# Kernel optimization log

Hardware: AMD Instinct MI355X
Metric: run time of the kernel (lower is better)

## Reference

```python
import jax, jax.numpy as jnp
import numpy as np

B, C, H, W = 8, 192, 56, 56
K = 9          # kernel_size (k nearest neighbors), dilation=1
G = 4          # conv groups in BasicConv
EPS_BN = 1e-5


def setup_inputs() -> dict:
    key = jax.random.key(0)
    ks = jax.random.split(key, 5)
    C2 = 2 * C
    gi = C2 // G
    x = jax.random.normal(ks[0], (B, C, H, W), jnp.float32)
    # fc1: Conv2d(C,C,1) + BN(C)
    w_fc1 = jax.random.normal(ks[1], (C, C), jnp.float32) * (1.0 / np.sqrt(C))
    b_fc1 = jnp.zeros((C,), jnp.float32)
    g_fc1 = jnp.ones((C,), jnp.float32)
    be_fc1 = jnp.zeros((C,), jnp.float32)
    # graph conv BasicConv: grouped Conv2d(2C,2C,1,groups=4) + BN(2C) + GELU
    w_gc = jax.random.normal(ks[2], (C2, gi), jnp.float32) * np.sqrt(2.0 / gi)  # kaiming
    b_gc = jnp.zeros((C2,), jnp.float32)
    g_gc = jnp.ones((C2,), jnp.float32)
    be_gc = jnp.zeros((C2,), jnp.float32)
    # fc2: Conv2d(2C,C,1) + BN(C)
    w_fc2 = jax.random.normal(ks[3], (C, C2), jnp.float32) * (1.0 / np.sqrt(C2))
    b_fc2 = jnp.zeros((C,), jnp.float32)
    g_fc2 = jnp.ones((C,), jnp.float32)
    be_fc2 = jnp.zeros((C,), jnp.float32)
    return dict(x=x, w_fc1=w_fc1, b_fc1=b_fc1, g_fc1=g_fc1, be_fc1=be_fc1,
                w_gc=w_gc, b_gc=b_gc, g_gc=g_gc, be_gc=be_gc,
                w_fc2=w_fc2, b_fc2=b_fc2, g_fc2=g_fc2, be_fc2=be_fc2)


def _bn(x, g, b):
    # training-mode BatchNorm over (batch, points) per channel; x: [B,N,C]
    mu = jnp.mean(x, axis=(0, 1))
    var = jnp.var(x, axis=(0, 1))  # biased, as torch BN uses for normalization
    return (x - mu) * jax.lax.rsqrt(var + EPS_BN) * g + b


def _forward(x, w_fc1, b_fc1, g_fc1, be_fc1, w_gc, b_gc, g_gc, be_gc,
             w_fc2, b_fc2, g_fc2, be_fc2):
    Bb, Cc, Hh, Ww = x.shape
    N = Hh * Ww
    x0 = x.reshape(Bb, Cc, N).transpose(0, 2, 1)          # [B,N,C]
    h = _bn(x0 @ w_fc1.T + b_fc1, g_fc1, be_fc1)          # fc1

    # --- dynamic kNN graph on L2-normalized features (no-grad in torch) ---
    f = jax.lax.stop_gradient(h)
    f = f / jnp.maximum(jnp.linalg.norm(f, axis=-1, keepdims=True), 1e-12)
    sq = jnp.sum(f * f, axis=-1, keepdims=True)           # [B,N,1]
    dist = sq - 2.0 * jnp.einsum('bnc,bmc->bnm', f, f) + sq.transpose(0, 2, 1)
    _, idx = jax.lax.top_k(-dist, K)                      # [B,N,K] neighbor indices

    # --- max-relative aggregation ---
    xj = h[jnp.arange(Bb)[:, None, None], idx]            # gather: [B,N,K,C]
    rel = jnp.max(xj - h[:, :, None, :], axis=2)          # [B,N,C]
    # interleave channels: c*2 + {0: h, 1: rel} (matches cat(dim=2).reshape)
    feat = jnp.stack([h, rel], axis=-1).reshape(Bb, N, 2 * Cc)

    # --- grouped 1x1 conv + BN + GELU ---
    C2 = 2 * Cc
    gi = C2 // G
    fg = feat.reshape(Bb, N, G, gi)
    wg = w_gc.reshape(G, gi, gi)                          # [group, out_pg, in_pg]
    y = jnp.einsum('bngi,goi->bngo', fg, wg).reshape(Bb, N, C2) + b_gc
    y = jax.nn.gelu(_bn(y, g_gc, be_gc), approximate=False)

    # --- fc2 + residual ---
    out = _bn(y @ w_fc2.T + b_fc2, g_fc2, be_fc2) + x0
    return out.transpose(0, 2, 1).reshape(Bb, Cc, Hh, Ww)


def reference(x, w_fc1, b_fc1, g_fc1, be_fc1, w_gc, b_gc, g_gc, be_gc,
              w_fc2, b_fc2, g_fc2, be_fc2):
    return _forward(x, w_fc1, b_fc1, g_fc1, be_fc1, w_gc, b_gc, g_gc, be_gc,
                    w_fc2, b_fc2, g_fc2, be_fc2)
```

## Files before the change

### kernel.cpp

```cpp
#include <hip/hip_runtime.h>
#include <math.h>

#define BB 8
#define CC 192
#define NN 3136
#define NR 25088
#define C2 384
#define GI 96
#define KNN 9
#define NCHUNK 256
#define RPC 98
#define EPS_BN 1e-5f

typedef unsigned short ushortT;
typedef unsigned int uintT;
typedef _Float16 f16x8 __attribute__((ext_vector_type(8)));
typedef float f32x4 __attribute__((ext_vector_type(4)));

static __device__ __forceinline__ ushortT f16b(_Float16 v) {
  union { _Float16 f; ushortT u; } x; x.f = v; return x.u;
}
static __device__ __forceinline__ float f16tof(ushortT u) {
  union { ushortT u; _Float16 f; } x; x.u = u; return (float)x.f;
}
static __device__ __forceinline__ float packdi(float d, int cidx) {
  return __uint_as_float((__float_as_uint(d) & 0xFFFFF800u) | (uintT)cidx);
}

__global__ __launch_bounds__(256) void k_fc1(const float* __restrict__ x,
        const float* __restrict__ w1, const float* __restrict__ b1,
        float* __restrict__ z) {
  __shared__ __align__(16) float Xs[32*68];
  __shared__ __align__(16) float Ws[32*68];
  int b = blockIdx.z, n0 = blockIdx.x*64, c0 = blockIdx.y*64;
  int tid = threadIdx.x;
  int tcol = tid & 15, trow = tid >> 4;
  float acc[4][4] = {};
  const float4* xf4 = (const float4*)x;
  const float4* wf4 = (const float4*)w1;
  for (int kb = 0; kb < 6; ++kb) {
    int k0 = kb*32;
    __syncthreads();
    #pragma unroll
    for (int s = 0; s < 2; ++s) {
      int q = tid + 256*s;
      int kk = q >> 4, nq = q & 15;
      ((float4*)Xs)[kk*17 + nq] = xf4[(size_t)(b*CC + k0 + kk)*784 + (n0>>2) + nq];
    }
    #pragma unroll
    for (int s = 0; s < 2; ++s) {
      int q = tid + 256*s;
      int cc = q >> 3, kq = q & 7;
      float4 v = wf4[(size_t)(c0 + cc)*48 + (k0>>2) + kq];
      Ws[(kq*4+0)*68 + cc] = v.x;
      Ws[(kq*4+1)*68 + cc] = v.y;
      Ws[(kq*4+2)*68 + cc] = v.z;
      Ws[(kq*4+3)*68 + cc] = v.w;
    }
    __syncthreads();
    #pragma unroll 8
    for (int kk = 0; kk < 32; ++kk) {
      float4 a4 = ((const float4*)Xs)[kk*17 + trow];
      float4 b4 = ((const float4*)Ws)[kk*17 + tcol];
      float av[4] = {a4.x,a4.y,a4.z,a4.w};
      float bv[4] = {b4.x,b4.y,b4.z,b4.w};
      #pragma unroll
      for (int i = 0; i < 4; ++i)
        #pragma unroll
        for (int j = 0; j < 4; ++j)
          acc[i][j] += av[i]*bv[j];
    }
  }
  float4 bias = ((const float4*)b1)[(c0>>2) + tcol];
  float bb4[4] = {bias.x,bias.y,bias.z,bias.w};
  #pragma unroll
  for (int i = 0; i < 4; ++i) {
    int n = n0 + trow*4 + i;
    float4 o;
    o.x = acc[i][0] + bb4[0]; o.y = acc[i][1] + bb4[1];
    o.z = acc[i][2] + bb4[2]; o.w = acc[i][3] + bb4[3];
    ((float4*)z)[(size_t)(b*NN + n)*48 + (c0>>2) + tcol] = o;
  }
}

__global__ void k_stats_part(const float* __restrict__ src, int C, float* __restrict__ part) {
  int c = threadIdx.x;
  int chunk = blockIdx.x;
  float s = 0.f, ss = 0.f;
  const float* p = src + (size_t)chunk*RPC*C + c;
  for (int r = 0; r < RPC; ++r) {
    float v = p[(size_t)r*C];
    s += v; ss += v*v;
  }
  part[(size_t)chunk*C + c] = s;
  part[(size_t)(NCHUNK + chunk)*C + c] = ss;
}

__global__ void k_stats_fin(const float* __restrict__ part, int C,
      const float* __restrict__ g, const float* __restrict__ be,
      float* __restrict__ scale, float* __restrict__ shift) {
  int c = threadIdx.x;
  float s = 0.f, ss = 0.f;
  for (int ch = 0; ch < NCHUNK; ++ch) {
    s  += part[(size_t)ch*C + c];
    ss += part[(size_t)(NCHUNK+ch)*C + c];
  }
  float mu = s / (float)NR;
  float var = ss/(float)NR - mu*mu;
  float rs = 1.0f / sqrtf(var + EPS_BN);
  float sc = g[c]*rs;
  scale[c] = sc;
  shift[c] = be[c] - mu*sc;
}

__global__ void k_packw(const float* __restrict__ src, int n4,
                        ushortT* __restrict__ hi, ushortT* __restrict__ lo) {
  int i = blockIdx.x*256 + threadIdx.x;
  if (i >= n4) return;
  float4 v = ((const float4*)src)[i];
  float vv[4] = {v.x, v.y, v.z, v.w};
  ushortT hb[4], lb[4];
  #pragma unroll
  for (int t = 0; t < 4; ++t) {
    _Float16 hh = (_Float16)vv[t];
    float r = vv[t] - (float)hh;
    _Float16 ll = (_Float16)(r*4096.f);
    hb[t] = f16b(hh); lb[t] = f16b(ll);
  }
  ((uint2*)hi)[i] = make_uint2((uintT)hb[0] | ((uintT)hb[1]<<16), (uintT)hb[2] | ((uintT)hb[3]<<16));
  ((uint2*)lo)[i] = make_uint2((uintT)lb[0] | ((uintT)lb[1]<<16), (uintT)lb[2] | ((uintT)lb[3]<<16));
}

__global__ __launch_bounds__(256) void k_h_f(float* __restrict__ h,
      ushortT* __restrict__ fhi, ushortT* __restrict__ flo, float* __restrict__ sqh,
      const float* __restrict__ scale, const float* __restrict__ shift) {
  __shared__ __align__(16) float fbuf[4][192];
  int w = threadIdx.x >> 6, lane = threadIdx.x & 63;
  size_t row = (size_t)blockIdx.x*4 + w;
  float* hp = h + row*CC;
  float hv[3]; float s = 0.f;
  #pragma unroll
  for (int t = 0; t < 3; ++t) {
    int c = lane + 64*t;
    float v = hp[c]*scale[c] + shift[c];
    hv[t] = v; s += v*v;
  }
  #pragma unroll
  for (int o = 32; o; o >>= 1) s += __shfl_xor(s, o);
  float eta = fmaxf(sqrtf(s), 1e-12f);
  float fv[3]; float s2 = 0.f;
  #pragma unroll
  for (int t = 0; t < 3; ++t) { fv[t] = hv[t]/eta; s2 += fv[t]*fv[t]; }
  #pragma unroll
  for (int o = 32; o; o >>= 1) s2 += __shfl_xor(s2, o);
  #pragma unroll
  for (int t = 0; t < 3; ++t) {
    int c = lane + 64*t;
    hp[c] = hv[t];
    fbuf[w][c] = fv[t];
  }
  if (lane == 0) sqh[row] = 0.5f*s2;
  __syncthreads();
  if (threadIdx.x < 192) {
    int r = threadIdx.x / 48, q = threadIdx.x % 48;
    size_t grow = (size_t)blockIdx.x*4 + r;
    float4 v = *(float4*)&fbuf[r][q*4];
    _Float16 a0=(_Float16)v.x, a1=(_Float16)v.y, a2=(_Float16)v.z, a3=(_Float16)v.w;
    float r0=v.x-(float)a0, r1=v.y-(float)a1, r2=v.z-(float)a2, r3=v.w-(float)a3;
    _Float16 b0=(_Float16)(r0*4096.f), b1=(_Float16)(r1*4096.f);
    _Float16 b2=(_Float16)(r2*4096.f), b3=(_Float16)(r3*4096.f);
    uintT hi0 = (uintT)f16b(a0) | ((uintT)f16b(a1)<<16);
    uintT hi1 = (uintT)f16b(a2) | ((uintT)f16b(a3)<<16);
    uintT lo0 = (uintT)f16b(b0) | ((uintT)f16b(b1)<<16);
    uintT lo1 = (uintT)f16b(b2) | ((uintT)f16b(b3)<<16);
    ((uint2*)(fhi + grow*CC))[q] = make_uint2(hi0, hi1);
    ((uint2*)(flo + grow*CC))[q] = make_uint2(lo0, lo1);
  }
}

__global__ __launch_bounds__(256) void k_knn12(const ushortT* __restrict__ fhi_,
    const float* __restrict__ sqh, int* __restrict__ idx12) {
  __shared__ __align__(16) f16x8 AHs[2][768];
  __shared__ float sqs[1568];
  int id = blockIdx.x;
  int b = id & 7, half = (id >> 3) & 1, rt = id >> 4;
  int tid = threadIdx.x, w = tid >> 6, lane = tid & 63;
  int l15 = lane & 15, kg = lane >> 4;

  const f16x8* FH = (const f16x8*)(fhi_ + (size_t)b*NN*CC);
  int cbase = half*1568;
  const f16x8* FC = FH + (size_t)cbase*24;

  int soff[3];
  #pragma unroll
  for (int i = 0; i < 3; ++i) {
    int s = i*256 + tid;
    int rr = s/24, u = s - rr*24;
    soff[i] = rr*24 + (u ^ (rr&7));
  }
  #pragma unroll
  for (int i = 0; i < 3; ++i)
    __builtin_amdgcn_global_load_lds(
      (const __attribute__((address_space(1))) void*)(FC + soff[i]),
      (__attribute__((address_space(3))) void*)&AHs[0][i*256 + w*64], 16, 0, 0);

  for (int i = tid; i < 1568/4; i += 256)
    ((float4*)sqs)[i] = ((const float4*)(sqh + (size_t)b*NN + cbase))[i];

  int row = rt*64 + w*16 + l15;
  f16x8 Bh[6];
  #pragma unroll
  for (int ks = 0; ks < 6; ++ks)
    Bh[ks] = FH[(size_t)row*24 + ks*4 + kg];

  float PD[12];
  #pragma unroll
  for (int t = 0; t < 12; ++t) PD[t] = -3.0e38f;

  __syncthreads();

  int buf = 0;
  for (int ct = 0; ct < 49; ++ct) {
    if (ct + 1 < 49) {
      #pragma unroll
      for (int i = 0; i < 3; ++i)
        __builtin_amdgcn_global_load_lds(
          (const __attribute__((address_space(1))) void*)(FC + (ct+1)*768 + soff[i]),
          (__attribute__((address_space(3))) void*)&AHs[buf^1][i*256 + w*64], 16, 0, 0);
    }
    f32x4 acc0 = {0.f,0.f,0.f,0.f}, acc1 = {0.f,0.f,0.f,0.f};
    #pragma unroll
    for (int ks = 0; ks < 6; ++ks) {
      int ub = ks*4 + kg;
      f16x8 a0 = AHs[buf][(     l15)*24 + (ub ^ (l15&7))];
      f16x8 a1 = AHs[buf][(16 + l15)*24 + (ub ^ (l15&7))];
      acc0 = __builtin_amdgcn_mfma_f32_16x16x32_f16(a0, Bh[ks], acc0, 0, 0, 0);
      acc1 = __builtin_amdgcn_mfma_f32_16x16x32_f16(a1, Bh[ks], acc1, 0, 0, 0);
    }
    int jbl = ct*32 + kg*4;
    float4 s0 = *(float4*)&sqs[jbl];
    float4 s1 = *(float4*)&sqs[jbl + 16];
    float dv[8] = {acc0[0]-s0.x, acc0[1]-s0.y, acc0[2]-s0.z, acc0[3]-s0.w,
                   acc1[0]-s1.x, acc1[1]-s1.y, acc1[2]-s1.z, acc1[3]-s1.w};
    #pragma unroll
    for (int r = 0; r < 8; ++r) {
      float dp = packdi(dv[r], jbl + (r&3) + ((r>>2)<<4));
      PD[0] = fmaxf(PD[0], dp);
      #pragma unroll
      for (int t = 0; t < 11; ++t) {
        float a = PD[t], c2 = PD[t+1];
        PD[t] = fminf(a, c2); PD[t+1] = fmaxf(a, c2);
      }
    }
    __syncthreads();
    buf ^= 1;
  }

  #pragma unroll
  for (int t = 0; t < 12; ++t) {
    float od = __shfl_xor(PD[t], 32);
    float od2 = (kg < 2) ? od : -3.0e38f;
    PD[0] = fmaxf(PD[0], od2);
    #pragma unroll
    for (int t2 = 0; t2 < 11; ++t2) {
      float a = PD[t2], c2 = PD[t2+1];
      PD[t2] = fminf(a, c2); PD[t2+1] = fmaxf(a, c2);
    }
  }
  #pragma unroll
  for (int t = 0; t < 12; ++t) {
    float od = __shfl_xor(PD[t], 16);
    float od2 = (kg == 0) ? od : -3.0e38f;
    PD[0] = fmaxf(PD[0], od2);
    #pragma unroll
    for (int t2 = 0; t2 < 11; ++t2) {
      float a = PD[t2], c2 = PD[t2+1];
      PD[t2] = fminf(a, c2); PD[t2+1] = fmaxf(a, c2);
    }
  }
  if (kg == 0) {
    size_t base = ((size_t)(b*NN + row)*2 + half)*12;
    #pragma unroll
    for (int t = 0; t < 12; ++t)
      idx12[base + t] = cbase + (int)(__float_as_uint(PD[t]) & 0x7FFu);
  }
}

__global__ __launch_bounds__(256) void k_refine(const ushortT* __restrict__ fhi_,
    const ushortT* __restrict__ flo_, const float* __restrict__ sqh,
    const int* __restrict__ idx12, int* __restrict__ idxg) {
  int id = blockIdx.x;
  int b = id & 7, rq = id >> 3;
  int w = threadIdx.x >> 6, lane = threadIdx.x & 63;
  int row = rq*4 + w;
  const ushortT* FHb = fhi_ + (size_t)b*NN*CC;
  const ushortT* FLb = flo_ + (size_t)b*NN*CC;
  float rv[3];
  #pragma unroll
  for (int t = 0; t < 3; ++t) {
    int c = lane + 64*t;
    rv[t] = f16tof(FHb[(size_t)row*CC + c]) + f16tof(FLb[(size_t)row*CC + c])*2.44140625e-4f;
  }
  const int* JP = idx12 + (size_t)(b*NN + row)*24;
  float TD[9]; int TI[9];
  #pragma unroll
  for (int t = 0; t < 9; ++t) { TD[t] = -3.0e38f; TI[t] = 0x7fffffff; }
  #pragma unroll
  for (int g = 0; g < 4; ++g) {
    int J6[6]; float s6[6];
    #pragma unroll
    for (int e = 0; e < 6; ++e) J6[e] = JP[g*6 + e];
    #pragma unroll
    for (int e = 0; e < 6; ++e) {
      int j = J6[e];
      float s = 0.f;
      #pragma unroll
      for (int t = 0; t < 3; ++t) {
        int c = lane + 64*t;
        float cv = f16tof(FHb[(size_t)j*CC + c]) + f16tof(FLb[(size_t)j*CC + c])*2.44140625e-4f;
        s = fmaf(rv[t], cv, s);
      }
      s6[e] = s;
    }
    #pragma unroll
    for (int o = 32; o; o >>= 1) {
      #pragma unroll
      for (int e = 0; e < 6; ++e) s6[e] += __shfl_xor(s6[e], o);
    }
    #pragma unroll
    for (int e = 0; e < 6; ++e) {
      int j = J6[e];
      float d = s6[e] - sqh[(size_t)b*NN + j];
      bool ins = (d > TD[0]) || (d == TD[0] && j < TI[0]);
      if (ins) {
        TD[0] = d; TI[0] = j;
        #pragma unroll
        for (int t = 0; t < 8; ++t) {
          bool sw = (TD[t] > TD[t+1]) || (TD[t] == TD[t+1] && TI[t] < TI[t+1]);
          if (sw) {
            float td = TD[t]; TD[t] = TD[t+1]; TD[t+1] = td;
            int ti = TI[t]; TI[t] = TI[t+1]; TI[t+1] = ti;
          }
        }
      }
    }
  }
  if (lane == 0) {
    size_t base = (size_t)(b*NN + row)*KNN;
    #pragma unroll
    for (int t = 0; t < KNN; ++t) idxg[base + t] = TI[t];
  }
}

__global__ __launch_bounds__(256) void k_gather(const float* __restrict__ h,
    const int* __restrict__ idxg, float* __restrict__ feat) {
  int w = threadIdx.x >> 6, lane = threadIdx.x & 63;
  size_t rg = (size_t)blockIdx.x*4 + w;
  int b = (int)(rg / NN);
  int n = (int)(rg % NN);
  const float* hb = h + (size_t)b*NN*CC;
  int j[KNN];
  #pragma unroll
  for (int t = 0; t < KNN; ++t) j[t] = idxg[rg*KNN + t];
  float2* featp = (float2*)feat;
  #pragma unroll
  for (int t = 0; t < 3; ++t) {
    int c = lane + 64*t;
    float self = hb[(size_t)n*CC + c];
    float m = -3.0e38f;
    #pragma unroll
    for (int k = 0; k < KNN; ++k) m = fmaxf(m, hb[(size_t)j[k]*CC + c]);
    featp[rg*CC + c] = make_float2(self, m - self);
  }
}

__global__ __launch_bounds__(256) void k_gconv(float* __restrict__ feat,
    const ushortT* __restrict__ wgh, const ushortT* __restrict__ wgl,
    const float* __restrict__ bgc, float* __restrict__ y) {
  int rt = blockIdx.x, g = blockIdx.y;
  int tid = threadIdx.x, w = tid >> 6, lane = tid & 63;
  int l15 = lane & 15, kg = lane >> 4;
  int row = rt*64 + w*16 + l15;
  const float4* F4 = (const float4*)feat;
  const f16x8* AH  = (const f16x8*)wgh;
  const f16x8* AL  = (const f16x8*)wgl;
  f16x8 Bh[3], Bl[3];
  #pragma unroll
  for (int ks = 0; ks < 3; ++ks) {
    float4 v0 = F4[(size_t)row*96 + g*24 + ks*8 + kg*2];
    float4 v1 = F4[(size_t)row*96 + g*24 + ks*8 + kg*2 + 1];
    float vv[8] = {v0.x,v0.y,v0.z,v0.w,v1.x,v1.y,v1.z,v1.w};
    #pragma unroll
    for (int e = 0; e < 8; ++e) {
      _Float16 hh = (_Float16)vv[e];
      Bh[ks][e] = hh;
      Bl[ks][e] = (_Float16)((vv[e] - (float)hh)*4096.f);
    }
  }
  #pragma unroll 3
  for (int nt = 0; nt < 6; ++nt) {
    f32x4 hh = {0.f,0.f,0.f,0.f}, hl = {0.f,0.f,0.f,0.f}, lh = {0.f,0.f,0.f,0.f};
    #pragma unroll
    for (int ks = 0; ks < 3; ++ks) {
      size_t au = (size_t)(g*GI + nt*16 + l15)*12 + ks*4 + kg;
      f16x8 Ah = AH[au], Al = AL[au];
      hh = __builtin_amdgcn_mfma_f32_16x16x32_f16(Ah, Bh[ks], hh, 0, 0, 0);
      hl = __builtin_amdgcn_mfma_f32_16x16x32_f16(Ah, Bl[ks], hl, 0, 0, 0);
      lh = __builtin_amdgcn_mfma_f32_16x16x32_f16(Al, Bh[ks], lh, 0, 0, 0);
    }
    float4 bias = ((const float4*)bgc)[g*24 + nt*4 + kg];
    float bb[4] = {bias.x, bias.y, bias.z, bias.w};
    float ov[4];
    #pragma unroll
    for (int r = 0; r < 4; ++r)
      ov[r] = fmaf(hl[r] + lh[r], 2.44140625e-4f, hh[r]) + bb[r];
    float4 o; o.x = ov[0]; o.y = ov[1]; o.z = ov[2]; o.w = ov[3];
    ((float4*)y)[(size_t)row*96 + g*24 + nt*4 + kg] = o;
  }
}

__global__ void k_bn_gelu(const float* __restrict__ y, ushortT* __restrict__ y2hi,
    ushortT* __restrict__ y2lo, const float* __restrict__ scale,
    const float* __restrict__ shift) {
  size_t i = (size_t)blockIdx.x*blockDim.x + threadIdx.x;
  float4 v = ((const float4*)y)[i];
  int c4 = (int)(i % 96);
  float4 sc = ((const float4*)scale)[c4], sh = ((const float4*)shift)[c4];
  float vv[4] = {v.x*sc.x+sh.x, v.y*sc.y+sh.y, v.z*sc.z+sh.z, v.w*sc.w+sh.w};
  ushortT hb[4], lb[4];
  #pragma unroll
  for (int t = 0; t < 4; ++t) {
    float g = 0.5f*vv[t]*(1.0f + erff(vv[t]*0.70710678118654752440f));
    _Float16 hh = (_Float16)g;
    float r = g - (float)hh;
    _Float16 ll = (_Float16)(r*4096.f);
    hb[t] = f16b(hh); lb[t] = f16b(ll);
  }
  ((uint2*)y2hi)[i] = make_uint2((uintT)hb[0] | ((uintT)hb[1]<<16), (uintT)hb[2] | ((uintT)hb[3]<<16));
  ((uint2*)y2lo)[i] = make_uint2((uintT)lb[0] | ((uintT)lb[1]<<16), (uintT)lb[2] | ((uintT)lb[3]<<16));
}

__global__ __launch_bounds__(256) void k_fc2(const ushortT* __restrict__ y2hi,
    const ushortT* __restrict__ y2lo, const ushortT* __restrict__ w2h,
    const ushortT* __restrict__ w2l, const float* __restrict__ b2, float* __restrict__ op) {
  int rt = blockIdx.x;
  int tid = threadIdx.x, w = tid >> 6, lane = tid & 63;
  int l15 = lane & 15, kg = lane >> 4;
  int row = rt*64 + w*16 + l15;
  const f16x8* YH = (const f16x8*)y2hi;
  const f16x8* YL = (const f16x8*)y2lo;
  const f16x8* AH = (const f16x8*)w2h;
  const f16x8* AL = (const f16x8*)w2l;
  f16x8 Bh[12], Bl[12];
  #pragma unroll
  for (int ks = 0; ks < 12; ++ks) {
    size_t u = (size_t)row*48 + ks*4 + kg;
    Bh[ks] = YH[u]; Bl[ks] = YL[u];
  }
  #pragma unroll 4
  for (int nt = 0; nt < 12; ++nt) {
    f32x4 hh = {0.f,0.f,0.f,0.f}, hl = {0.f,0.f,0.f,0.f}, lh = {0.f,0.f,0.f,0.f};
    #pragma unroll
    for (int ks = 0; ks < 12; ++ks) {
      size_t au = (size_t)(nt*16 + l15)*48 + ks*4 + kg;
      f16x8 Ah = AH[au], Al = AL[au];
      hh = __builtin_amdgcn_mfma_f32_16x16x32_f16(Ah, Bh[ks], hh, 0, 0, 0);
      hl = __builtin_amdgcn_mfma_f32_16x16x32_f16(Ah, Bl[ks], hl, 0, 0, 0);
      lh = __builtin_amdgcn_mfma_f32_16x16x32_f16(Al, Bh[ks], lh, 0, 0, 0);
    }
    float4 bias = ((const float4*)b2)[nt*4 + kg];
    float bb[4] = {bias.x, bias.y, bias.z, bias.w};
    float ov[4];
    #pragma unroll
    for (int r = 0; r < 4; ++r)
      ov[r] = fmaf(hl[r] + lh[r], 2.44140625e-4f, hh[r]) + bb[r];
    float4 o; o.x = ov[0]; o.y = ov[1]; o.z = ov[2]; o.w = ov[3];
    ((float4*)op)[(size_t)row*48 + nt*4 + kg] = o;
  }
}

__global__ __launch_bounds__(256) void k_final(const float* __restrict__ op,
    const float* __restrict__ x, const float* __restrict__ scale,
    const float* __restrict__ shift, float* __restrict__ out) {
  __shared__ float t[32][33];
  int n0 = blockIdx.x*32, c0 = blockIdx.y*32, b = blockIdx.z;
  int tx = threadIdx.x, ty = threadIdx.y;
  #pragma unroll
  for (int s = 0; s < 4; ++s) {
    int r = ty + 8*s;
    int c = c0 + tx;
    t[r][tx] = op[((size_t)b*NN + n0 + r)*CC + c]*scale[c] + shift[c];
  }
  __syncthreads();
  #pragma unroll
  for (int s = 0; s < 4; ++s) {
    int c = ty + 8*s;
    size_t o = ((size_t)b*CC + c0 + c)*NN + n0 + tx;
    out[o] = t[tx][c] + x[o];
  }
}

extern "C" void kernel_launch(void* const* d_in, const int* in_sizes, int n_in,
                              void* d_out, int out_size, void* d_ws, size_t ws_size,
                              hipStream_t stream) {
  (void)in_sizes; (void)n_in; (void)out_size; (void)ws_size;
  const float* x   = (const float*)d_in[0];
  const float* w1  = (const float*)d_in[1];
  const float* b1  = (const float*)d_in[2];
  const float* g1  = (const float*)d_in[3];
  const float* be1 = (const float*)d_in[4];
  const float* wgc = (const float*)d_in[5];
  const float* bgc = (const float*)d_in[6];
  const float* g2  = (const float*)d_in[7];
  const float* be2 = (const float*)d_in[8];
  const float* w2  = (const float*)d_in[9];
  const float* b2  = (const float*)d_in[10];
  const float* g3  = (const float*)d_in[11];
  const float* be3 = (const float*)d_in[12];
  float* ws = (float*)d_ws;

  float* h      = ws;
  ushortT* fhi  = (ushortT*)(ws + 4816896);
  ushortT* flo  = (ushortT*)(ws + 7225344);
  float* feat   = ws + 4816896;
  float* y      = feat;
  ushortT* y2hi = (ushortT*)ws;
  ushortT* y2lo = (ushortT*)(ws + 14450688);
  float* op     = ws + 4816896;
  float* sqh    = ws + 14450688;
  int*   idxg   = (int*)(ws + 14475776);
  int*   idx12  = (int*)(ws + 14701568);
  float* st     = ws + 19267584;
  float* part   = ws + 19269120;
  ushortT* w2h  = (ushortT*)(ws + 19465728);
  ushortT* w2l  = (ushortT*)(ws + 19502592);
  ushortT* wgh  = (ushortT*)(ws + 19539456);
  ushortT* wgl  = (ushortT*)(ws + 19557888);
  float* sc1 = st;        float* sh1 = st + 192;
  float* sc2 = st + 384;  float* sh2 = st + 768;
  float* sc3 = st + 1152; float* sh3 = st + 1344;
  float* out = (float*)d_out;

  k_packw<<<72, 256, 0, stream>>>(w2, 18432, w2h, w2l);
  k_packw<<<36, 256, 0, stream>>>(wgc, 9216, wgh, wgl);
  k_fc1<<<dim3(49,3,8), 256, 0, stream>>>(x, w1, b1, h);
  k_stats_part<<<NCHUNK, CC, 0, stream>>>(h, CC, part);
  k_stats_fin<<<1, CC, 0, stream>>>(part, CC, g1, be1, sc1, sh1);
  k_h_f<<<NR/4, 256, 0, stream>>>(h, fhi, flo, sqh, sc1, sh1);
  k_knn12<<<dim3(784), 256, 0, stream>>>(fhi, sqh, idx12);
  k_refine<<<dim3(6272), 256, 0, stream>>>(fhi, flo, sqh, idx12, idxg);
  k_gather<<<NR/4, 256, 0, stream>>>(h, idxg, feat);
  k_gconv<<<dim3(392,4), 256, 0, stream>>>(feat, wgh, wgl, bgc, y);
  k_stats_part<<<NCHUNK, C2, 0, stream>>>(y, C2, part);
  k_stats_fin<<<1, C2, 0, stream>>>(part, C2, g2, be2, sc2, sh2);
  k_bn_gelu<<<9408, 256, 0, stream>>>(y, y2hi, y2lo, sc2, sh2);
  k_fc2<<<dim3(392), 256, 0, stream>>>(y2hi, y2lo, w2h, w2l, b2, op);
  k_stats_part<<<NCHUNK, CC, 0, stream>>>(op, CC, part);
  k_stats_fin<<<1, CC, 0, stream>>>(part, CC, g3, be3, sc3, sh3);
  k_final<<<dim3(98,6,8), dim3(32,8), 0, stream>>>(op, x, sc3, sh3, out);
}
```

Baseline: 518.9 us.

## Move fc1 to split-fp16 MFMA and fuse BN stats finalize via atomic ticket

Replaces the scalar FP32 tiled fc1 GEMM with an MFMA kernel that uses a hi/lo fp16 split (three MFMAs per step). A new transpose-and-pack kernel converts x into that split format first. Weight packing is merged into one launch, and each BN stats partial/finalize pair becomes a single kernel where the last block, found through an atomic ticket, does the finalize. This trades an extra pass over x and some precision risk for tensor-core throughput and fewer launches.

```diff
diff --git a/kernel.cpp b/kernel.cpp
--- a/kernel.cpp
+++ b/kernel.cpp
@@ -26,64 +26,119 @@
 static __device__ __forceinline__ float packdi(float d, int cidx) {
   return __uint_as_float((__float_as_uint(d) & 0xFFFFF800u) | (uintT)cidx);
 }
-
-__global__ __launch_bounds__(256) void k_fc1(const float* __restrict__ x,
-        const float* __restrict__ w1, const float* __restrict__ b1,
-        float* __restrict__ z) {
-  __shared__ __align__(16) float Xs[32*68];
-  __shared__ __align__(16) float Ws[32*68];
-  int b = blockIdx.z, n0 = blockIdx.x*64, c0 = blockIdx.y*64;
+static __device__ __forceinline__ void split8(const float* vv, f16x8& hi, f16x8& lo) {
+  #pragma unroll
+  for (int e = 0; e < 8; ++e) {
+    _Float16 hh = (_Float16)vv[e];
+    hi[e] = hh;
+    lo[e] = (_Float16)((vv[e] - (float)hh)*4096.f);
+  }
+}
+
+__global__ void k_pack(const float* __restrict__ w1, const float* __restrict__ w2,
+    const float* __restrict__ wgc,
+    ushortT* __restrict__ w1h, ushortT* __restrict__ w1l,
+    ushortT* __restrict__ w2h, ushortT* __restrict__ w2l,
+    ushortT* __restrict__ wgh, ushortT* __restrict__ wgl, int* __restrict__ ticket) {
+  int i = blockIdx.x*256 + threadIdx.x;
+  if (blockIdx.x == 0 && threadIdx.x < 3) ticket[threadIdx.x] = 0;
+  const float* src; ushortT* hi; ushortT* lo; int k;
+  if (i < 9216)        { src = w1;  hi = w1h; lo = w1l; k = i; }
+  else if (i < 27648)  { src = w2;  hi = w2h; lo = w2l; k = i - 9216; }
+  else if (i < 36864)  { src = wgc; hi = wgh; lo = wgl; k = i - 27648; }
+  else return;
+  float4 v = ((const float4*)src)[k];
+  float vv[4] = {v.x, v.y, v.z, v.w};
+  ushortT hb[4], lb[4];
+  #pragma unroll
+  for (int t = 0; t < 4; ++t) {
+    _Float16 hh = (_Float16)vv[t];
+    float r = vv[t] - (float)hh;
+    hb[t] = f16b(hh); lb[t] = f16b((_Float16)(r*4096.f));
+  }
+  ((uint2*)hi)[k] = make_uint2((uintT)hb[0] | ((uintT)hb[1]<<16), (uintT)hb[2] | ((uintT)hb[3]<<16));
+  ((uint2*)lo)[k] = make_uint2((uintT)lb[0] | ((uintT)lb[1]<<16), (uintT)lb[2] | ((uintT)lb[3]<<16));
+}
+
+__global__ __launch_bounds__(256) void k_packx(const float* __restrict__ x,
+    ushortT* __restrict__ xhi, ushortT* __restrict__ xlo) {
+  __shared__ float Ls[192][33];
+  int b = blockIdx.y, n0 = blockIdx.x*32;
   int tid = threadIdx.x;
-  int tcol = tid & 15, trow = tid >> 4;
-  float acc[4][4] = {};
-  const float4* xf4 = (const float4*)x;
-  const float4* wf4 = (const float4*)w1;
-  for (int kb = 0; kb < 6; ++kb) {
-    int k0 = kb*32;
-    __syncthreads();
-    #pragma unroll
-    for (int s = 0; s < 2; ++s) {
-      int q = tid + 256*s;
-      int kk = q >> 4, nq = q & 15;
-      ((float4*)Xs)[kk*17 + nq] = xf4[(size_t)(b*CC + k0 + kk)*784 + (n0>>2) + nq];
-    }
-    #pragma unroll
-    for (int s = 0; s < 2; ++s) {
-      int q = tid + 256*s;
-      int cc = q >> 3, kq = q & 7;
-      float4 v = wf4[(size_t)(c0 + cc)*48 + (k0>>2) + kq];
-      Ws[(kq*4+0)*68 + cc] = v.x;
-      Ws[(kq*4+1)*68 + cc] = v.y;
-      Ws[(kq*4+2)*68 + cc] = v.z;
-      Ws[(kq*4+3)*68 + cc] = v.w;
-    }
-    __syncthreads();
-    #pragma unroll 8
-    for (int kk = 0; kk < 32; ++kk) {
-      float4 a4 = ((const float4*)Xs)[kk*17 + trow];
-      float4 b4 = ((const float4*)Ws)[kk*17 + tcol];
-      float av[4] = {a4.x,a4.y,a4.z,a4.w};
-      float bv[4] = {b4.x,b4.y,b4.z,b4.w};
-      #pragma unroll
-      for (int i = 0; i < 4; ++i)
-        #pragma unroll
-        for (int j = 0; j < 4; ++j)
-          acc[i][j] += av[i]*bv[j];
-    }
-  }
-  float4 bias = ((const float4*)b1)[(c0>>2) + tcol];
-  float bb4[4] = {bias.x,bias.y,bias.z,bias.w};
-  #pragma unroll
-  for (int i = 0; i < 4; ++i) {
-    int n = n0 + trow*4 + i;
-    float4 o;
-    o.x = acc[i][0] + bb4[0]; o.y = acc[i][1] + bb4[1];
-    o.z = acc[i][2] + bb4[2]; o.w = acc[i][3] + bb4[3];
-    ((float4*)z)[(size_t)(b*NN + n)*48 + (c0>>2) + tcol] = o;
-  }
-}
-
-__global__ void k_stats_part(const float* __restrict__ src, int C, float* __restrict__ part) {
+  int tn = tid & 31, tc0 = tid >> 5;
+  #pragma unroll
+  for (int i = 0; i < 24; ++i) {
+    int c = tc0 + 8*i;
+    Ls[c][tn] = x[((size_t)(b*CC + c))*NN + n0 + tn];
+  }
+  __syncthreads();
+  #pragma unroll
+  for (int i = 0; i < 3; ++i) {
+    int t = tid + 256*i;
+    int n = t / 24, u = t - n*24;
+    float vv[8];
+    #pragma unroll
+    for (int e = 0; e < 8; ++e) vv[e] = Ls[u*8 + e][n];
+    ushortT hb[8], lb[8];
+    #pragma unroll
+    for (int e = 0; e < 8; ++e) {
+      _Float16 hh = (_Float16)vv[e];
+      hb[e] = f16b(hh);
+      lb[e] = f16b((_Float16)((vv[e] - (float)hh)*4096.f));
+    }
+    size_t row = (size_t)b*NN + n0 + n;
+    uint4 hq, lq;
+    hq.x = (uintT)hb[0]|((uintT)hb[1]<<16); hq.y = (uintT)hb[2]|((uintT)hb[3]<<16);
+    hq.z = (uintT)hb[4]|((uintT)hb[5]<<16); hq.w = (uintT)hb[6]|((uintT)hb[7]<<16);
+    lq.x = (uintT)lb[0]|((uintT)lb[1]<<16); lq.y = (uintT)lb[2]|((uintT)lb[3]<<16);
+    lq.z = (uintT)lb[4]|((uintT)lb[5]<<16); lq.w = (uintT)lb[6]|((uintT)lb[7]<<16);
+    ((uint4*)xhi)[row*24 + u] = hq;
+    ((uint4*)xlo)[row*24 + u] = lq;
+  }
+}
+
+__global__ __launch_bounds__(256) void k_fc1m(const ushortT* __restrict__ xhi,
+    const ushortT* __restrict__ xlo, const ushortT* __restrict__ w1h,
+    const ushortT* __restrict__ w1l, const float* __restrict__ b1, float* __restrict__ z) {
+  int rt = blockIdx.x;
+  int tid = threadIdx.x, w = tid >> 6, lane = tid & 63;
+  int l15 = lane & 15, kg = lane >> 4;
+  int row = rt*64 + w*16 + l15;
+  const f16x8* XH = (const f16x8*)xhi;
+  const f16x8* XL = (const f16x8*)xlo;
+  const f16x8* AH = (const f16x8*)w1h;
+  const f16x8* AL = (const f16x8*)w1l;
+  f16x8 Bh[6], Bl[6];
+  #pragma unroll
+  for (int ks = 0; ks < 6; ++ks) {
+    size_t u = (size_t)row*24 + ks*4 + kg;
+    Bh[ks] = XH[u]; Bl[ks] = XL[u];
+  }
+  #pragma unroll 4
+  for (int nt = 0; nt < 12; ++nt) {
+    f32x4 hh = {0.f,0.f,0.f,0.f}, hl = {0.f,0.f,0.f,0.f}, lh = {0.f,0.f,0.f,0.f};
+    #pragma unroll
+    for (int ks = 0; ks < 6; ++ks) {
+      size_t au = (size_t)(nt*16 + l15)*24 + ks*4 + kg;
+      f16x8 Ah = AH[au], Al = AL[au];
+      hh = __builtin_amdgcn_mfma_f32_16x16x32_f16(Ah, Bh[ks], hh, 0, 0, 0);
+      hl = __builtin_amdgcn_mfma_f32_16x16x32_f16(Ah, Bl[ks], hl, 0, 0, 0);
+      lh = __builtin_amdgcn_mfma_f32_16x16x32_f16(Al, Bh[ks], lh, 0, 0, 0);
+    }
+    float4 bias = ((const float4*)b1)[nt*4 + kg];
+    float bb[4] = {bias.x, bias.y, bias.z, bias.w};
+    float ov[4];
+    #pragma unroll
+    for (int r = 0; r < 4; ++r)
+      ov[r] = fmaf(hl[r] + lh[r], 2.44140625e-4f, hh[r]) + bb[r];
+    float4 o; o.x = ov[0]; o.y = ov[1]; o.z = ov[2]; o.w = ov[3];
+    ((float4*)z)[(size_t)row*48 + nt*4 + kg] = o;
+  }
+}
+
+__global__ void k_stats(const float* __restrict__ src, int C, float* __restrict__ part,
+      const float* __restrict__ g, const float* __restrict__ be,
+      float* __restrict__ scale, float* __restrict__ shift, int* __restrict__ ticket) {
   int c = threadIdx.x;
   int chunk = blockIdx.x;
   float s = 0.f, ss = 0.f;
@@ -94,41 +149,24 @@
   }
   part[(size_t)chunk*C + c] = s;
   part[(size_t)(NCHUNK + chunk)*C + c] = ss;
-}
-
-__global__ void k_stats_fin(const float* __restrict__ part, int C,
-      const float* __restrict__ g, const float* __restrict__ be,
-      float* __restrict__ scale, float* __restrict__ shift) {
-  int c = threadIdx.x;
-  float s = 0.f, ss = 0.f;
-  for (int ch = 0; ch < NCHUNK; ++ch) {
-    s  += part[(size_t)ch*C + c];
-    ss += part[(size_t)(NCHUNK+ch)*C + c];
-  }
-  float mu = s / (float)NR;
-  float var = ss/(float)NR - mu*mu;
-  float rs = 1.0f / sqrtf(var + EPS_BN);
-  float sc = g[c]*rs;
-  scale[c] = sc;
-  shift[c] = be[c] - mu*sc;
-}
-
-__global__ void k_packw(const float* __restrict__ src, int n4,
-                        ushortT* __restrict__ hi, ushortT* __restrict__ lo) {
-  int i = blockIdx.x*256 + threadIdx.x;
-  if (i >= n4) return;
-  float4 v = ((const float4*)src)[i];
-  float vv[4] = {v.x, v.y, v.z, v.w};
-  ushortT hb[4], lb[4];
-  #pragma unroll
-  for (int t = 0; t < 4; ++t) {
-    _Float16 hh = (_Float16)vv[t];
-    float r = vv[t] - (float)hh;
-    _Float16 ll = (_Float16)(r*4096.f);
-    hb[t] = f16b(hh); lb[t] = f16b(ll);
-  }
-  ((uint2*)hi)[i] = make_uint2((uintT)hb[0] | ((uintT)hb[1]<<16), (uintT)hb[2] | ((uintT)hb[3]<<16));
-  ((uint2*)lo)[i] = make_uint2((uintT)lb[0] | ((uintT)lb[1]<<16), (uintT)lb[2] | ((uintT)lb[3]<<16));
+  __threadfence();
+  __shared__ int islast;
+  if (c == 0) islast = (atomicAdd(ticket, 1) == NCHUNK-1);
+  __syncthreads();
+  if (islast) {
+    __threadfence();
+    float s2 = 0.f, ss2 = 0.f;
+    for (int ch = 0; ch < NCHUNK; ++ch) {
+      s2  += part[(size_t)ch*C + c];
+      ss2 += part[(size_t)(NCHUNK+ch)*C + c];
+    }
+    float mu = s2 / (float)NR;
+    float var = ss2/(float)NR - mu*mu;
+    float rs = 1.0f / sqrtf(var + EPS_BN);
+    float sc = g[c]*rs;
+    scale[c] = sc;
+    shift[c] = be[c] - mu*sc;
+  }
 }
 
 __global__ __launch_bounds__(256) void k_h_f(float* __restrict__ h,
@@ -390,12 +428,7 @@
     float4 v0 = F4[(size_t)row*96 + g*24 + ks*8 + kg*2];
     float4 v1 = F4[(size_t)row*96 + g*24 + ks*8 + kg*2 + 1];
     float vv[8] = {v0.x,v0.y,v0.z,v0.w,v1.x,v1.y,v1.z,v1.w};
-    #pragma unroll
-    for (int e = 0; e < 8; ++e) {
-      _Float16 hh = (_Float16)vv[e];
-      Bh[ks][e] = hh;
-      Bl[ks][e] = (_Float16)((vv[e] - (float)hh)*4096.f);
-    }
+    split8(vv, Bh[ks], Bl[ks]);
   }
   #pragma unroll 3
   for (int nt = 0; nt < 6; ++nt) {
@@ -433,8 +466,7 @@
     float g = 0.5f*vv[t]*(1.0f + erff(vv[t]*0.70710678118654752440f));
     _Float16 hh = (_Float16)g;
     float r = g - (float)hh;
-    _Float16 ll = (_Float16)(r*4096.f);
-    hb[t] = f16b(hh); lb[t] = f16b(ll);
+    hb[t] = f16b(hh); lb[t] = f16b((_Float16)(r*4096.f));
   }
   ((uint2*)y2hi)[i] = make_uint2((uintT)hb[0] | ((uintT)hb[1]<<16), (uintT)hb[2] | ((uintT)hb[3]<<16));
   ((uint2*)y2lo)[i] = make_uint2((uintT)lb[0] | ((uintT)lb[1]<<16), (uintT)lb[2] | ((uintT)lb[3]<<16));
@@ -520,6 +552,8 @@
   float* ws = (float*)d_ws;
 
   float* h      = ws;
+  ushortT* xhi  = (ushortT*)(ws + 4816896);
+  ushortT* xlo  = (ushortT*)(ws + 7225344);
   ushortT* fhi  = (ushortT*)(ws + 4816896);
   ushortT* flo  = (ushortT*)(ws + 7225344);
   float* feat   = ws + 4816896;
@@ -536,26 +570,26 @@
   ushortT* w2l  = (ushortT*)(ws + 19502592);
   ushortT* wgh  = (ushortT*)(ws + 19539456);
   ushortT* wgl  = (ushortT*)(ws + 19557888);
+  ushortT* w1h  = (ushortT*)(ws + 19576320);
+  ushortT* w1l  = (ushortT*)(ws + 19613184);
+  int* tickets  = (int*)(ws + 19650048);
   float* sc1 = st;        float* sh1 = st + 192;
   float* sc2 = st + 384;  float* sh2 = st + 768;
   float* sc3 = st + 1152; float* sh3 = st + 1344;
   float* out = (float*)d_out;
 
-  k_packw<<<72, 256, 0, stream>>>(w2, 18432, w2h, w2l);
-  k_packw<<<36, 256, 0, stream>>>(wgc, 9216, wgh, wgl);
-  k_fc1<<<dim3(49,3,8), 256, 0, stream>>>(x, w1, b1, h);
-  k_stats_part<<<NCHUNK, CC, 0, stream>>>(h, CC, part);
-  k_stats_fin<<<1, CC, 0, stream>>>(part, CC, g1, be1, sc1, sh1);
+  k_pack<<<144, 256, 0, stream>>>(w1, w2, wgc, w1h, w1l, w2h, w2l, wgh, wgl, tickets);
+  k_packx<<<dim3(98,8), 256, 0, stream>>>(x, xhi, xlo);
+  k_fc1m<<<392, 256, 0, stream>>>(xhi, xlo, w1h, w1l, b1, h);
+  k_stats<<<NCHUNK, CC, 0, stream>>>(h, CC, part, g1, be1, sc1, sh1, tickets + 0);
   k_h_f<<<NR/4, 256, 0, stream>>>(h, fhi, flo, sqh, sc1, sh1);
   k_knn12<<<dim3(784), 256, 0, stream>>>(fhi, sqh, idx12);
   k_refine<<<dim3(6272), 256, 0, stream>>>(fhi, flo, sqh, idx12, idxg);
   k_gather<<<NR/4, 256, 0, stream>>>(h, idxg, feat);
   k_gconv<<<dim3(392,4), 256, 0, stream>>>(feat, wgh, wgl, bgc, y);
-  k_stats_part<<<NCHUNK, C2, 0, stream>>>(y, C2, part);
-  k_stats_fin<<<1, C2, 0, stream>>>(part, C2, g2, be2, sc2, sh2);
+  k_stats<<<NCHUNK, C2, 0, stream>>>(y, C2, part, g2, be2, sc2, sh2, tickets + 1);
   k_bn_gelu<<<9408, 256, 0, stream>>>(y, y2hi, y2lo, sc2, sh2);
-  k_fc2<<<dim3(392), 256, 0, stream>>>(y2hi, y2lo, w2h, w2l, b2, op);
-  k_stats_part<<<NCHUNK, CC, 0, stream>>>(op, CC, part);
-  k_stats_fin<<<1, CC, 0, stream>>>(part, CC, g3, be3, sc3, sh3);
+  k_fc2<<<392, 256, 0, stream>>>(y2hi, y2lo, w2h, w2l, b2, op);
+  k_stats<<<NCHUNK, CC, 0, stream>>>(op, CC, part, g3, be3, sc3, sh3, tickets + 2);
   k_final<<<dim3(98,6,8), dim3(32,8), 0, stream>>>(op, x, sc3, sh3, out);
 }
```

Measured after the change: 586.5 us. 13.0% more time.
